# Kernel optimization log

Measured on AMD Instinct MI355X. Metric: run time of the kernel, lower is better.

## Reference

```python
import jax, jax.numpy as jnp
import numpy as np

B, H, S, D = 2, 16, 2048, 64


def setup_inputs() -> dict:
    key = jax.random.key(0)
    kq, kk, kv = jax.random.split(key, 3)
    q = jax.random.normal(kq, (B, H, S, D), dtype=jnp.float32)
    k = jax.random.normal(kk, (B, H, S, D), dtype=jnp.float32)
    v = jax.random.normal(kv, (B, H, S, D), dtype=jnp.float32)
    # causal mask: 1.0 where attention is DISALLOWED (strictly upper triangle)
    mask = jnp.triu(jnp.ones((S, S), dtype=jnp.float32), k=1)[None, None, :, :]
    return {"k": k, "q": q, "v": v, "mask": mask}


def reference(k, q, v, mask):
    d_k = jnp.asarray(k.shape[-1], dtype=jnp.float32)
    # scores: [B, H, S, S]
    scores = jnp.einsum("bhqd,bhkd->bhqk", q, k) / jnp.sqrt(d_k)
    scores = scores + mask * (-1e9)
    weights = jax.nn.softmax(scores, axis=-1)
    # attention output: [B, H, S, D]
    return jnp.einsum("bhqk,bhkd->bhqd", weights, v)
```

## Files before the change

kernel.cpp:

```cpp
#include <hip/hip_runtime.h>
#include <hip/hip_bf16.h>

typedef unsigned short ushort_t;
typedef __attribute__((ext_vector_type(8))) short v8s;
typedef __attribute__((ext_vector_type(4))) float v4f;

#define SEQ   2048
#define DH    64
#define BK    32
#define KSTR  72
#define VSTR  40

#if __has_builtin(__builtin_amdgcn_exp2f)
#define EXP2(x) __builtin_amdgcn_exp2f(x)
#else
#define EXP2(x) exp2f(x)
#endif

__device__ __forceinline__ unsigned pkbf(float lo, float hi) {
    __hip_bfloat162 h = __float22bfloat162_rn(make_float2(lo, hi));
    union { __hip_bfloat162 h; unsigned u; } c; c.h = h; return c.u;
}

__device__ __forceinline__ v8s load8_bf_scaled(const float* p, float sc) {
    float4 a = *(const float4*)p;
    float4 b = *(const float4*)(p + 4);
    union { v8s v; unsigned u[4]; } t;
    t.u[0] = pkbf(a.x * sc, a.y * sc);
    t.u[1] = pkbf(a.z * sc, a.w * sc);
    t.u[2] = pkbf(b.x * sc, b.y * sc);
    t.u[3] = pkbf(b.z * sc, b.w * sc);
    return t.v;
}

__device__ __forceinline__ void process_tile_T(
    int kb, int myq0, int quad, int l15,
    v8s qa0, v8s qa1,
    v8s ka00, v8s ka01, v8s ka10, v8s ka11,
    v8s vb0, v8s vb1, v8s vb2, v8s vb3,
    v4f& a0, v4f& a1, v4f& a2, v4f& a3, float& ls)
{
    const v4f z = {0.f, 0.f, 0.f, 0.f};
    __builtin_amdgcn_s_setprio(1);
    v4f s0 = __builtin_amdgcn_mfma_f32_16x16x32_bf16(ka00, qa0, z, 0, 0, 0);
    s0     = __builtin_amdgcn_mfma_f32_16x16x32_bf16(ka01, qa1, s0, 0, 0, 0);
    v4f s1 = __builtin_amdgcn_mfma_f32_16x16x32_bf16(ka10, qa0, z, 0, 0, 0);
    s1     = __builtin_amdgcn_mfma_f32_16x16x32_bf16(ka11, qa1, s1, 0, 0, 0);
    __builtin_amdgcn_s_setprio(0);

    float p0[4], p1[4];
    if (kb + BK <= myq0) {
        #pragma unroll
        for (int r = 0; r < 4; ++r) { p0[r] = EXP2(s0[r]); p1[r] = EXP2(s1[r]); }
    } else {
        const int qrow = myq0 + l15;
        #pragma unroll
        for (int r = 0; r < 4; ++r) {
            p0[r] = (kb + 4 * quad + r      <= qrow) ? EXP2(s0[r]) : 0.f;
            p1[r] = (kb + 16 + 4 * quad + r <= qrow) ? EXP2(s1[r]) : 0.f;
        }
    }
    #pragma unroll
    for (int r = 0; r < 4; ++r) ls += p0[r] + p1[r];

    union { v8s v; unsigned u[4]; } pa;
    pa.u[0] = pkbf(p0[0], p0[1]); pa.u[1] = pkbf(p0[2], p0[3]);
    pa.u[2] = pkbf(p1[0], p1[1]); pa.u[3] = pkbf(p1[2], p1[3]);
    __builtin_amdgcn_s_setprio(1);
    a0 = __builtin_amdgcn_mfma_f32_16x16x32_bf16(pa.v, vb0, a0, 0, 0, 0);
    a1 = __builtin_amdgcn_mfma_f32_16x16x32_bf16(pa.v, vb1, a1, 0, 0, 0);
    a2 = __builtin_amdgcn_mfma_f32_16x16x32_bf16(pa.v, vb2, a2, 0, 0, 0);
    a3 = __builtin_amdgcn_mfma_f32_16x16x32_bf16(pa.v, vb3, a3, 0, 0, 0);
    __builtin_amdgcn_s_setprio(0);
}

__global__ __launch_bounds__(256, 4)
void attn_causal_kernel(const float* __restrict__ Kg,
                        const float* __restrict__ Qg,
                        const float* __restrict__ Vg,
                        float* __restrict__ Og) {
    __shared__ alignas(16) ushort_t Kt[2][BK * KSTR];
    __shared__ alignas(16) ushort_t Vt[2][DH * VSTR];

    const int i    = blockIdx.x;
    const int head = i & 31;
    const int qt   = 31 - (i >> 5);
    const int qb   = qt * 64;
    const int tid  = threadIdx.x;
    const int w    = tid >> 6;
    const int lane = tid & 63;
    const int l15  = lane & 15;
    const int quad = lane >> 4;

    const int myq0 = qb + w * 16, qmax = myq0 + 15;
    const size_t hb = (size_t)head * SEQ * DH;

    const float QSC = 0.125f * 1.4426950408889634f;
    v8s qa0, qa1;
    {
        const float* qp = Qg + hb + (size_t)(myq0 + l15) * DH + quad * 8;
        qa0 = load8_bf_scaled(qp, QSC);  qa1 = load8_bf_scaled(qp + 32, QSC);
    }

    v4f a0 = {0.f,0.f,0.f,0.f}, a1 = a0, a2 = a0, a3 = a0;
    float ls = 0.f;

    const int ntiles = (qb + 64) / BK;

    const int sk_kpos = tid >> 3;
    const int sk_d    = (tid & 7) * 8;
    const int sv_d = tid & 63;

    const float* kbase  = Kg + hb + (size_t)sk_kpos * DH + sk_d;
    const float* vbaseA = Vg + hb + (size_t)(4 * w) * DH + sv_d;
    const float* vbaseB = Vg + hb + (size_t)(16 + 4 * w) * DH + sv_d;
    ushort_t* kdst0 = &Kt[0][sk_kpos * KSTR + sk_d];
    ushort_t* vdst0 = &Vt[0][sv_d * VSTR + 8 * w];
    const int KOFS = BK * KSTR;
    const int VOFS = DH * VSTR;

    {
        float4 k0 = *(const float4*)(kbase);
        float4 k1 = *(const float4*)(kbase + 4);
        float va[4], vb[4];
        #pragma unroll
        for (int m = 0; m < 4; ++m) {
            va[m] = vbaseA[(size_t)m * DH];
            vb[m] = vbaseB[(size_t)m * DH];
        }
        union { v8s v; unsigned u[4]; } kc, vc;
        kc.u[0] = pkbf(k0.x, k0.y); kc.u[1] = pkbf(k0.z, k0.w);
        kc.u[2] = pkbf(k1.x, k1.y); kc.u[3] = pkbf(k1.z, k1.w);
        vc.u[0] = pkbf(va[0], va[1]); vc.u[1] = pkbf(va[2], va[3]);
        vc.u[2] = pkbf(vb[0], vb[1]); vc.u[3] = pkbf(vb[2], vb[3]);
        *(v8s*)kdst0 = kc.v;
        *(v8s*)vdst0 = vc.v;
    }
    __syncthreads();

    for (int kt = 0; kt < ntiles; ++kt) {
        const int cur = kt & 1;
        const bool havenext = (kt + 1 < ntiles);

        float4 nk0, nk1; float nva[4], nvb[4];
        if (havenext) {
            const size_t toff = (size_t)(kt + 1) * BK * DH;
            nk0 = *(const float4*)(kbase + toff);
            nk1 = *(const float4*)(kbase + toff + 4);
            #pragma unroll
            for (int m = 0; m < 4; ++m) {
                nva[m] = vbaseA[toff + (size_t)m * DH];
                nvb[m] = vbaseB[toff + (size_t)m * DH];
            }
        }

        const int kb = kt * BK;
        if (kb <= qmax) {
            const ushort_t* KB = &Kt[0][cur ? KOFS : 0];
            const ushort_t* VB = &Vt[0][cur ? VOFS : 0];
            union { v8s v; uint4 u; } ka00, ka01, ka10, ka11, vb0, vb1, vb2, vb3;
            ka00.u = *(const uint4*)&KB[(l15)      * KSTR      + quad * 8];
            ka01.u = *(const uint4*)&KB[(l15)      * KSTR + 32 + quad * 8];
            ka10.u = *(const uint4*)&KB[(16 + l15) * KSTR      + quad * 8];
            ka11.u = *(const uint4*)&KB[(16 + l15) * KSTR + 32 + quad * 8];
            vb0.u  = *(const uint4*)&VB[(l15)      * VSTR + quad * 8];
            vb1.u  = *(const uint4*)&VB[(16 + l15) * VSTR + quad * 8];
            vb2.u  = *(const uint4*)&VB[(32 + l15) * VSTR + quad * 8];
            vb3.u  = *(const uint4*)&VB[(48 + l15) * VSTR + quad * 8];

            process_tile_T(kb, myq0, quad, l15, qa0, qa1,
                           ka00.v, ka01.v, ka10.v, ka11.v,
                           vb0.v, vb1.v, vb2.v, vb3.v,
                           a0, a1, a2, a3, ls);
        }

        if (havenext) {
            union { v8s v; unsigned u[4]; } kc, vc;
            kc.u[0] = pkbf(nk0.x, nk0.y); kc.u[1] = pkbf(nk0.z, nk0.w);
            kc.u[2] = pkbf(nk1.x, nk1.y); kc.u[3] = pkbf(nk1.z, nk1.w);
            vc.u[0] = pkbf(nva[0], nva[1]); vc.u[1] = pkbf(nva[2], nva[3]);
            vc.u[2] = pkbf(nvb[0], nvb[1]); vc.u[3] = pkbf(nvb[2], nvb[3]);
            const int nxt = cur ^ 1;
            *(v8s*)(kdst0 + (nxt ? KOFS : 0)) = kc.v;
            *(v8s*)(vdst0 + (nxt ? VOFS : 0)) = vc.v;
        }

        __syncthreads();
    }

    ls += __shfl_xor(ls, 16); ls += __shfl_xor(ls, 32);

    #pragma unroll
    for (int r = 0; r < 4; ++r) {
        const float inv = 1.0f / __shfl(ls, 4 * quad + r);
        float* op = Og + hb + (size_t)(myq0 + 4 * quad + r) * DH + l15;
        op[0]  = a0[r] * inv; op[16] = a1[r] * inv;
        op[32] = a2[r] * inv; op[48] = a3[r] * inv;
    }
}

extern "C" void kernel_launch(void* const* d_in, const int* in_sizes, int n_in,
                              void* d_out, int out_size, void* d_ws, size_t ws_size,
                              hipStream_t stream) {
    const float* K = (const float*)d_in[0];
    const float* Q = (const float*)d_in[1];
    const float* V = (const float*)d_in[2];
    float* O = (float*)d_out;
    attn_causal_kernel<<<dim3(1024), 256, 0, stream>>>(K, Q, V, O);
}
```

Before: 142.7 us.

## Split causal KV range across two blocks and combine partial sums

Each query tile's key range is split into two halves handled by separate blocks, which doubles the grid to 2048 blocks and raises the occupancy hint to 8. Unnormalized partial outputs and row sums go to the output and a workspace buffer, and a second kernel adds them and normalizes. The aim is better load balance and occupancy for the causal triangle, at the cost of an extra kernel launch and extra global traffic for the partials. If the workspace is too small, the code falls back to the original single kernel.

```diff
diff --git a/kernel.cpp b/kernel.cpp
--- a/kernel.cpp
+++ b/kernel.cpp
@@ -10,6 +10,7 @@
 #define BK    32
 #define KSTR  72
 #define VSTR  40
+#define NHEADS 32
 
 #if __has_builtin(__builtin_amdgcn_exp2f)
 #define EXP2(x) __builtin_amdgcn_exp2f(x)
@@ -74,17 +75,21 @@
     __builtin_amdgcn_s_setprio(0);
 }
 
-__global__ __launch_bounds__(256, 4)
-void attn_causal_kernel(const float* __restrict__ Kg,
-                        const float* __restrict__ Qg,
-                        const float* __restrict__ Vg,
-                        float* __restrict__ Og) {
+__global__ __launch_bounds__(256, 8)
+void attn_causal_split(const float* __restrict__ Kg,
+                       const float* __restrict__ Qg,
+                       const float* __restrict__ Vg,
+                       float* __restrict__ Og,
+                       float* __restrict__ A1,
+                       float* __restrict__ Ls) {
     __shared__ alignas(16) ushort_t Kt[2][BK * KSTR];
     __shared__ alignas(16) ushort_t Vt[2][DH * VSTR];
 
     const int i    = blockIdx.x;
     const int head = i & 31;
-    const int qt   = 31 - (i >> 5);
+    const int rest = i >> 5;
+    const int qt   = 31 - (rest >> 1);
+    const int half = rest & 1;
     const int qb   = qt * 64;
     const int tid  = threadIdx.x;
     const int w    = tid >> 6;
@@ -92,6 +97,9 @@
     const int l15  = lane & 15;
     const int quad = lane >> 4;
 
+    const int ktlo = half ? (qt + 1) : 0;
+    const int kthi = half ? (2 * qt + 2) : (qt + 1);
+
     const int myq0 = qb + w * 16, qmax = myq0 + 15;
     const size_t hb = (size_t)head * SEQ * DH;
 
@@ -104,8 +112,6 @@
 
     v4f a0 = {0.f,0.f,0.f,0.f}, a1 = a0, a2 = a0, a3 = a0;
     float ls = 0.f;
-
-    const int ntiles = (qb + 64) / BK;
 
     const int sk_kpos = tid >> 3;
     const int sk_d    = (tid & 7) * 8;
@@ -120,13 +126,14 @@
     const int VOFS = DH * VSTR;
 
     {
-        float4 k0 = *(const float4*)(kbase);
-        float4 k1 = *(const float4*)(kbase + 4);
+        const size_t t0 = (size_t)ktlo * BK * DH;
+        float4 k0 = *(const float4*)(kbase + t0);
+        float4 k1 = *(const float4*)(kbase + t0 + 4);
         float va[4], vb[4];
         #pragma unroll
         for (int m = 0; m < 4; ++m) {
-            va[m] = vbaseA[(size_t)m * DH];
-            vb[m] = vbaseB[(size_t)m * DH];
+            va[m] = vbaseA[t0 + (size_t)m * DH];
+            vb[m] = vbaseB[t0 + (size_t)m * DH];
         }
         union { v8s v; unsigned u[4]; } kc, vc;
         kc.u[0] = pkbf(k0.x, k0.y); kc.u[1] = pkbf(k0.z, k0.w);
@@ -138,9 +145,9 @@
     }
     __syncthreads();
 
-    for (int kt = 0; kt < ntiles; ++kt) {
-        const int cur = kt & 1;
-        const bool havenext = (kt + 1 < ntiles);
+    for (int kt = ktlo; kt < kthi; ++kt) {
+        const int cur = (kt - ktlo) & 1;
+        const bool havenext = (kt + 1 < kthi);
 
         float4 nk0, nk1; float nva[4], nvb[4];
         if (havenext) {
@@ -190,6 +197,154 @@
 
     ls += __shfl_xor(ls, 16); ls += __shfl_xor(ls, 32);
 
+    float* lsrow = Ls + ((size_t)half * NHEADS + head) * SEQ;
+    if (lane < 16) lsrow[myq0 + l15] = ls;
+
+    float* Ab = (half ? A1 : Og) + hb;
+    #pragma unroll
+    for (int r = 0; r < 4; ++r) {
+        float* op = Ab + (size_t)(myq0 + 4 * quad + r) * DH + l15;
+        op[0]  = a0[r]; op[16] = a1[r];
+        op[32] = a2[r]; op[48] = a3[r];
+    }
+}
+
+__global__ __launch_bounds__(256, 8)
+void attn_combine(float* __restrict__ Og,
+                  const float* __restrict__ A1,
+                  const float* __restrict__ Ls) {
+    const size_t nv4 = (size_t)NHEADS * SEQ * DH / 4;
+    const float* ls0 = Ls;
+    const float* ls1 = Ls + (size_t)NHEADS * SEQ;
+    for (size_t idx = (size_t)blockIdx.x * blockDim.x + threadIdx.x;
+         idx < nv4; idx += (size_t)gridDim.x * blockDim.x) {
+        const size_t row = idx >> 4;
+        float4 o = ((const float4*)Og)[idx];
+        float4 a = ((const float4*)A1)[idx];
+        const float inv = 1.0f / (ls0[row] + ls1[row]);
+        float4 r;
+        r.x = (o.x + a.x) * inv; r.y = (o.y + a.y) * inv;
+        r.z = (o.z + a.z) * inv; r.w = (o.w + a.w) * inv;
+        ((float4*)Og)[idx] = r;
+    }
+}
+
+__global__ __launch_bounds__(256, 4)
+void attn_causal_mono(const float* __restrict__ Kg,
+                      const float* __restrict__ Qg,
+                      const float* __restrict__ Vg,
+                      float* __restrict__ Og) {
+    __shared__ alignas(16) ushort_t Kt[2][BK * KSTR];
+    __shared__ alignas(16) ushort_t Vt[2][DH * VSTR];
+
+    const int i    = blockIdx.x;
+    const int head = i & 31;
+    const int qt   = 31 - (i >> 5);
+    const int qb   = qt * 64;
+    const int tid  = threadIdx.x;
+    const int w    = tid >> 6;
+    const int lane = tid & 63;
+    const int l15  = lane & 15;
+    const int quad = lane >> 4;
+
+    const int myq0 = qb + w * 16, qmax = myq0 + 15;
+    const size_t hb = (size_t)head * SEQ * DH;
+
+    const float QSC = 0.125f * 1.4426950408889634f;
+    v8s qa0, qa1;
+    {
+        const float* qp = Qg + hb + (size_t)(myq0 + l15) * DH + quad * 8;
+        qa0 = load8_bf_scaled(qp, QSC);  qa1 = load8_bf_scaled(qp + 32, QSC);
+    }
+
+    v4f a0 = {0.f,0.f,0.f,0.f}, a1 = a0, a2 = a0, a3 = a0;
+    float ls = 0.f;
+
+    const int ntiles = (qb + 64) / BK;
+
+    const int sk_kpos = tid >> 3;
+    const int sk_d    = (tid & 7) * 8;
+    const int sv_d = tid & 63;
+
+    const float* kbase  = Kg + hb + (size_t)sk_kpos * DH + sk_d;
+    const float* vbaseA = Vg + hb + (size_t)(4 * w) * DH + sv_d;
+    const float* vbaseB = Vg + hb + (size_t)(16 + 4 * w) * DH + sv_d;
+    ushort_t* kdst0 = &Kt[0][sk_kpos * KSTR + sk_d];
+    ushort_t* vdst0 = &Vt[0][sv_d * VSTR + 8 * w];
+    const int KOFS = BK * KSTR;
+    const int VOFS = DH * VSTR;
+
+    {
+        float4 k0 = *(const float4*)(kbase);
+        float4 k1 = *(const float4*)(kbase + 4);
+        float va[4], vb[4];
+        #pragma unroll
+        for (int m = 0; m < 4; ++m) {
+            va[m] = vbaseA[(size_t)m * DH];
+            vb[m] = vbaseB[(size_t)m * DH];
+        }
+        union { v8s v; unsigned u[4]; } kc, vc;
+        kc.u[0] = pkbf(k0.x, k0.y); kc.u[1] = pkbf(k0.z, k0.w);
+        kc.u[2] = pkbf(k1.x, k1.y); kc.u[3] = pkbf(k1.z, k1.w);
+        vc.u[0] = pkbf(va[0], va[1]); vc.u[1] = pkbf(va[2], va[3]);
+        vc.u[2] = pkbf(vb[0], vb[1]); vc.u[3] = pkbf(vb[2], vb[3]);
+        *(v8s*)kdst0 = kc.v;
+        *(v8s*)vdst0 = vc.v;
+    }
+    __syncthreads();
+
+    for (int kt = 0; kt < ntiles; ++kt) {
+        const int cur = kt & 1;
+        const bool havenext = (kt + 1 < ntiles);
+
+        float4 nk0, nk1; float nva[4], nvb[4];
+        if (havenext) {
+            const size_t toff = (size_t)(kt + 1) * BK * DH;
+            nk0 = *(const float4*)(kbase + toff);
+            nk1 = *(const float4*)(kbase + toff + 4);
+            #pragma unroll
+            for (int m = 0; m < 4; ++m) {
+                nva[m] = vbaseA[toff + (size_t)m * DH];
+                nvb[m] = vbaseB[toff + (size_t)m * DH];
+            }
+        }
+
+        const int kb = kt * BK;
+        if (kb <= qmax) {
+            const ushort_t* KB = &Kt[0][cur ? KOFS : 0];
+            const ushort_t* VB = &Vt[0][cur ? VOFS : 0];
+            union { v8s v; uint4 u; } ka00, ka01, ka10, ka11, vb0, vb1, vb2, vb3;
+            ka00.u = *(const uint4*)&KB[(l15)      * KSTR      + quad * 8];
+            ka01.u = *(const uint4*)&KB[(l15)      * KSTR + 32 + quad * 8];
+            ka10.u = *(const uint4*)&KB[(16 + l15) * KSTR      + quad * 8];
+            ka11.u = *(const uint4*)&KB[(16 + l15) * KSTR + 32 + quad * 8];
+            vb0.u  = *(const uint4*)&VB[(l15)      * VSTR + quad * 8];
+            vb1.u  = *(const uint4*)&VB[(16 + l15) * VSTR + quad * 8];
+            vb2.u  = *(const uint4*)&VB[(32 + l15) * VSTR + quad * 8];
+            vb3.u  = *(const uint4*)&VB[(48 + l15) * VSTR + quad * 8];
+
+            process_tile_T(kb, myq0, quad, l15, qa0, qa1,
+                           ka00.v, ka01.v, ka10.v, ka11.v,
+                           vb0.v, vb1.v, vb2.v, vb3.v,
+                           a0, a1, a2, a3, ls);
+        }
+
+        if (havenext) {
+            union { v8s v; unsigned u[4]; } kc, vc;
+            kc.u[0] = pkbf(nk0.x, nk0.y); kc.u[1] = pkbf(nk0.z, nk0.w);
+            kc.u[2] = pkbf(nk1.x, nk1.y); kc.u[3] = pkbf(nk1.z, nk1.w);
+            vc.u[0] = pkbf(nva[0], nva[1]); vc.u[1] = pkbf(nva[2], nva[3]);
+            vc.u[2] = pkbf(nvb[0], nvb[1]); vc.u[3] = pkbf(nvb[2], nvb[3]);
+            const int nxt = cur ^ 1;
+            *(v8s*)(kdst0 + (nxt ? KOFS : 0)) = kc.v;
+            *(v8s*)(vdst0 + (nxt ? VOFS : 0)) = vc.v;
+        }
+
+        __syncthreads();
+    }
+
+    ls += __shfl_xor(ls, 16); ls += __shfl_xor(ls, 32);
+
     #pragma unroll
     for (int r = 0; r < 4; ++r) {
         const float inv = 1.0f / __shfl(ls, 4 * quad + r);
@@ -206,5 +361,17 @@
     const float* Q = (const float*)d_in[1];
     const float* V = (const float*)d_in[2];
     float* O = (float*)d_out;
-    attn_causal_kernel<<<dim3(1024), 256, 0, stream>>>(K, Q, V, O);
-}
+
+    const size_t a1_elems = (size_t)NHEADS * SEQ * DH;
+    const size_t ls_elems = (size_t)2 * NHEADS * SEQ;
+    const size_t need = (a1_elems + ls_elems) * sizeof(float);
+
+    if (ws_size >= need) {
+        float* A1 = (float*)d_ws;
+        float* Ls = A1 + a1_elems;
+        attn_causal_split<<<dim3(2048), 256, 0, stream>>>(K, Q, V, O, A1, Ls);
+        attn_combine<<<dim3(1024), 256, 0, stream>>>(O, A1, Ls);
+    } else {
+        attn_causal_mono<<<dim3(1024), 256, 0, stream>>>(K, Q, V, O);
+    }
+}
```

Result: slower. 500.5 us (+250.8%).

## Split KV range across two wave groups per block and merge partial outputs

Applied to the files above, without the earlier changes.

Each block now runs 512 threads as two groups of four waves. Each group streams half of the causal key/value tiles into its own double-buffered shared-memory region. Group 1 writes its partial output and row sums to shared memory, and group 0 adds them in before normalizing and storing. The q-tile ordering also changes so long and short tiles interleave across blockIdx, meant to shorten the per-block serial KV loop and improve load balance. The cost is more shared memory per block, a final merge step with an extra barrier, and possibly lower occupancy. Merging without a running max is valid only because the original code also uses no max subtraction.

```diff
diff --git a/kernel.cpp b/kernel.cpp
--- a/kernel.cpp
+++ b/kernel.cpp
@@ -10,6 +10,8 @@
 #define BK    32
 #define KSTR  72
 #define VSTR  40
+#define NHEADS 32
+#define GBYTES 19456
 
 #if __has_builtin(__builtin_amdgcn_exp2f)
 #define EXP2(x) __builtin_amdgcn_exp2f(x)
@@ -74,25 +76,30 @@
     __builtin_amdgcn_s_setprio(0);
 }
 
-__global__ __launch_bounds__(256, 4)
-void attn_causal_kernel(const float* __restrict__ Kg,
-                        const float* __restrict__ Qg,
-                        const float* __restrict__ Vg,
-                        float* __restrict__ Og) {
-    __shared__ alignas(16) ushort_t Kt[2][BK * KSTR];
-    __shared__ alignas(16) ushort_t Vt[2][DH * VSTR];
+__global__ __launch_bounds__(512, 4)
+void attn_causal_dual(const float* __restrict__ Kg,
+                      const float* __restrict__ Qg,
+                      const float* __restrict__ Vg,
+                      float* __restrict__ Og) {
+    __shared__ alignas(16) unsigned char smem[2][GBYTES];
 
     const int i    = blockIdx.x;
     const int head = i & 31;
-    const int qt   = 31 - (i >> 5);
+    const int j    = i >> 5;
+    const int qt   = (j < 16) ? (31 - j) : (j - 16);
     const int qb   = qt * 64;
     const int tid  = threadIdx.x;
     const int w    = tid >> 6;
+    const int grp  = w >> 2;
+    const int wg   = w & 3;
     const int lane = tid & 63;
     const int l15  = lane & 15;
     const int quad = lane >> 4;
 
-    const int myq0 = qb + w * 16, qmax = myq0 + 15;
+    const int niter = qt + 1;
+    const int ktlo  = grp ? niter : 0;
+
+    const int myq0 = qb + wg * 16, qmax = myq0 + 15;
     const size_t hb = (size_t)head * SEQ * DH;
 
     const float QSC = 0.125f * 1.4426950408889634f;
@@ -105,28 +112,31 @@
     v4f a0 = {0.f,0.f,0.f,0.f}, a1 = a0, a2 = a0, a3 = a0;
     float ls = 0.f;
 
-    const int ntiles = (qb + 64) / BK;
-
-    const int sk_kpos = tid >> 3;
-    const int sk_d    = (tid & 7) * 8;
-    const int sv_d = tid & 63;
+    const int stid    = tid & 255;
+    const int sk_kpos = stid >> 3;
+    const int sk_d    = (stid & 7) * 8;
+    const int sv_d    = stid & 63;
 
     const float* kbase  = Kg + hb + (size_t)sk_kpos * DH + sk_d;
-    const float* vbaseA = Vg + hb + (size_t)(4 * w) * DH + sv_d;
-    const float* vbaseB = Vg + hb + (size_t)(16 + 4 * w) * DH + sv_d;
-    ushort_t* kdst0 = &Kt[0][sk_kpos * KSTR + sk_d];
-    ushort_t* vdst0 = &Vt[0][sv_d * VSTR + 8 * w];
+    const float* vbaseA = Vg + hb + (size_t)(4 * wg) * DH + sv_d;
+    const float* vbaseB = Vg + hb + (size_t)(16 + 4 * wg) * DH + sv_d;
+
+    ushort_t* KtB = (ushort_t*)(smem[grp]);
+    ushort_t* VtB = (ushort_t*)(smem[grp] + 9216);
+    ushort_t* kdst0 = KtB + sk_kpos * KSTR + sk_d;
+    ushort_t* vdst0 = VtB + sv_d * VSTR + 8 * wg;
     const int KOFS = BK * KSTR;
     const int VOFS = DH * VSTR;
 
     {
-        float4 k0 = *(const float4*)(kbase);
-        float4 k1 = *(const float4*)(kbase + 4);
+        const size_t t0 = (size_t)ktlo * BK * DH;
+        float4 k0 = *(const float4*)(kbase + t0);
+        float4 k1 = *(const float4*)(kbase + t0 + 4);
         float va[4], vb[4];
         #pragma unroll
         for (int m = 0; m < 4; ++m) {
-            va[m] = vbaseA[(size_t)m * DH];
-            vb[m] = vbaseB[(size_t)m * DH];
+            va[m] = vbaseA[t0 + (size_t)m * DH];
+            vb[m] = vbaseB[t0 + (size_t)m * DH];
         }
         union { v8s v; unsigned u[4]; } kc, vc;
         kc.u[0] = pkbf(k0.x, k0.y); kc.u[1] = pkbf(k0.z, k0.w);
@@ -138,9 +148,10 @@
     }
     __syncthreads();
 
-    for (int kt = 0; kt < ntiles; ++kt) {
-        const int cur = kt & 1;
-        const bool havenext = (kt + 1 < ntiles);
+    for (int it = 0; it < niter; ++it) {
+        const int kt  = ktlo + it;
+        const int cur = it & 1;
+        const bool havenext = (it + 1 < niter);
 
         float4 nk0, nk1; float nva[4], nvb[4];
         if (havenext) {
@@ -156,8 +167,8 @@
 
         const int kb = kt * BK;
         if (kb <= qmax) {
-            const ushort_t* KB = &Kt[0][cur ? KOFS : 0];
-            const ushort_t* VB = &Vt[0][cur ? VOFS : 0];
+            const ushort_t* KB = KtB + (cur ? KOFS : 0);
+            const ushort_t* VB = VtB + (cur ? VOFS : 0);
             union { v8s v; uint4 u; } ka00, ka01, ka10, ka11, vb0, vb1, vb2, vb3;
             ka00.u = *(const uint4*)&KB[(l15)      * KSTR      + quad * 8];
             ka01.u = *(const uint4*)&KB[(l15)      * KSTR + 32 + quad * 8];
@@ -190,12 +201,31 @@
 
     ls += __shfl_xor(ls, 16); ls += __shfl_xor(ls, 32);
 
-    #pragma unroll
-    for (int r = 0; r < 4; ++r) {
-        const float inv = 1.0f / __shfl(ls, 4 * quad + r);
-        float* op = Og + hb + (size_t)(myq0 + 4 * quad + r) * DH + l15;
-        op[0]  = a0[r] * inv; op[16] = a1[r] * inv;
-        op[32] = a2[r] * inv; op[48] = a3[r] * inv;
+    float* Ps = (float*)smem[0];
+    float* Lp = (float*)smem[1];
+    if (grp == 1) {
+        #pragma unroll
+        for (int r = 0; r < 4; ++r) {
+            const int row = wg * 16 + 4 * quad + r;
+            float* pr = Ps + row * 68 + l15;
+            pr[0] = a0[r]; pr[16] = a1[r]; pr[32] = a2[r]; pr[48] = a3[r];
+        }
+        if (lane < 16) Lp[wg * 16 + l15] = ls;
+    }
+    __syncthreads();
+    if (grp == 0) {
+        const float lst = ls + Lp[wg * 16 + l15];
+        #pragma unroll
+        for (int r = 0; r < 4; ++r) {
+            const float inv = 1.0f / __shfl(lst, 4 * quad + r);
+            const int row = wg * 16 + 4 * quad + r;
+            const float* pr = Ps + row * 68 + l15;
+            float* op = Og + hb + (size_t)(qb + row) * DH + l15;
+            op[0]  = (a0[r] + pr[0])  * inv;
+            op[16] = (a1[r] + pr[16]) * inv;
+            op[32] = (a2[r] + pr[32]) * inv;
+            op[48] = (a3[r] + pr[48]) * inv;
+        }
     }
 }
 
@@ -206,5 +236,5 @@
     const float* Q = (const float*)d_in[1];
     const float* V = (const float*)d_in[2];
     float* O = (float*)d_out;
-    attn_causal_kernel<<<dim3(1024), 256, 0, stream>>>(K, Q, V, O);
-}
+    attn_causal_dual<<<dim3(1024), 512, 0, stream>>>(K, Q, V, O);
+}
```

New measurement: 142.1 us. No clear change (-0.4%).
